# Performance work log

Measured on AMD Instinct MI355X. Metric: run time of the kernel, lower is better.

The kernel has to match this reference:

```python
import jax, jax.numpy as jnp
import numpy as np

H = 4096          # hidden_size (Llama-3.1-8B)
BLK = 32          # sca_block_size
NB = H // BLK     # 128 blocks
R = 4             # sca_block_rank
K = 3             # sca_top_k
SIGMA = 1.0       # sca_sigma
NUM_TASKS = 10


def setup_inputs() -> dict:
    key = jax.random.key(0)
    ks = jax.random.split(key, 9)
    B, S = 4, 4096
    x = jax.random.normal(ks[0], (B, S, H), jnp.float32)
    task_ids = jax.random.randint(ks[1], (B,), 0, NUM_TASKS)
    task_emb = jax.random.normal(ks[2], (NUM_TASKS, H), jnp.float32) * 0.02
    Wp = jax.random.normal(ks[3], (H, 3), jnp.float32) * (1.0 / np.sqrt(H))  # spatial_proj (xavier-ish)
    bp = jnp.zeros((3,), jnp.float32)
    centers = jax.random.normal(ks[4], (NB, 3), jnp.float32)                 # block_centers
    A = jax.random.normal(ks[5], (NB, H, R), jnp.float32) * 0.02             # per-block down proj
    Bm = jax.random.normal(ks[6], (NB, R, BLK), jnp.float32) * 0.02          # per-block up proj into its hidden slice
    adapter_scale = jnp.float32(1.0)
    return dict(x=x, task_ids=task_ids, task_emb=task_emb, Wp=Wp, bp=bp,
                centers=centers, A=A, Bm=Bm, adapter_scale=adapter_scale)


def reference(x, task_ids, task_emb, Wp, bp, centers, A, Bm, adapter_scale):
    # task conditioning
    h = x + task_emb[task_ids][:, None, :]                     # [B,S,H]
    # spatial routing: project tokens to 3D, Gaussian score vs block centers
    coords = h @ Wp + bp                                       # [B,S,3]
    d2 = jnp.sum((coords[:, :, None, :] - centers[None, None]) ** 2, axis=-1)  # [B,S,NB]
    scores = -d2 / (2.0 * SIGMA ** 2)
    top_s, top_i = jax.lax.top_k(scores, K)                    # [B,S,K]
    gates = jax.nn.softmax(top_s, axis=-1)                     # soft mask over selected blocks
    # low-rank adapter per block (dense spmm_impl): down-project against all blocks, gather top-k
    z = jnp.einsum('bsh,nhr->bsnr', h, A)                      # [B,S,NB,R]
    z_sel = jnp.take_along_axis(z, top_i[..., None], axis=2)   # [B,S,K,R]
    B_sel = Bm[top_i]                                          # [B,S,K,R,BLK]
    delta_blk = jnp.einsum('bskr,bskrc->bskc', z_sel, B_sel) * gates[..., None]  # [B,S,K,BLK]
    # scatter block outputs into their hidden slices
    Bn, Sn = x.shape[0], x.shape[1]
    cols = top_i[..., None] * BLK + jnp.arange(BLK)            # [B,S,K,BLK]
    bi = jnp.arange(Bn)[:, None, None, None]
    si = jnp.arange(Sn)[None, :, None, None]
    delta = jnp.zeros_like(x).at[bi, si, cols].add(delta_blk)  # [B,S,H]
    return x + adapter_scale * delta
```

## Files before the change

### kernel.cpp

```cpp
#include <hip/hip_runtime.h>
#include <math.h>

#define HDIM 4096
#define NBLK 128
#define RNK  4
#define TOPK 3

typedef float f4 __attribute__((ext_vector_type(4)));
typedef float f2 __attribute__((ext_vector_type(2)));
typedef _Float16 h8 __attribute__((ext_vector_type(8)));

__global__ __launch_bounds__(256) void convert_A(
    const float* __restrict__ A, _Float16* __restrict__ Ah)
{
    int i = blockIdx.x * 256 + threadIdx.x;
    const f4* src = reinterpret_cast<const f4*>(A);
    f4 a0 = __builtin_nontemporal_load(src + 2 * i);
    f4 a1 = __builtin_nontemporal_load(src + 2 * i + 1);
    h8 r;
    r[0] = (_Float16)a0.x; r[1] = (_Float16)a0.y;
    r[2] = (_Float16)a0.z; r[3] = (_Float16)a0.w;
    r[4] = (_Float16)a1.x; r[5] = (_Float16)a1.y;
    r[6] = (_Float16)a1.z; r[7] = (_Float16)a1.w;
    reinterpret_cast<h8*>(Ah)[i] = r;
}

template<bool FP16A>
__global__ __launch_bounds__(256) void npl_fused(
    const float* __restrict__ x,
    const int*   __restrict__ task_ids,
    const float* __restrict__ task_emb,
    const float* __restrict__ Wp,
    const float* __restrict__ bp,
    const float* __restrict__ centers,
    const float* __restrict__ A,
    const _Float16* __restrict__ Ah,
    const float* __restrict__ Bm,
    const float* __restrict__ scale_p,
    float* __restrict__ out,
    int S_per_batch)
{
    __shared__ float h_lds[HDIM];
    __shared__ float red[4][16];
    __shared__ float sc[NBLK];
    __shared__ float zf[TOPK * RNK];
    __shared__ int   top_i[TOPK];
    __shared__ float gate[TOPK];
    __shared__ float dblk[TOPK * 32];
    __shared__ float coords_s[3];

    const int tid  = threadIdx.x;
    const int wid  = tid >> 6;
    const int lane = tid & 63;
    const int token = blockIdx.x;
    const int b = token / S_per_batch;
    const int task = task_ids[b];

    const float* xrow = x + (size_t)token * HDIM;
    const float* trow = task_emb + (size_t)task * HDIM;
    float*       orow = out + (size_t)token * HDIM;

    const f4* xr4 = reinterpret_cast<const f4*>(xrow);
    const f4* tr4 = reinterpret_cast<const f4*>(trow);
    f4*       or4 = reinterpret_cast<f4*>(orow);

    f4 xv[4];
    float c0 = 0.f, c1 = 0.f, c2 = 0.f;
#pragma unroll
    for (int k = 0; k < 4; ++k) {
        int i4 = tid + k * 256;
        f4 xx = __builtin_nontemporal_load(xr4 + i4);
        f4 tt = tr4[i4];
        xv[k] = xx;
        f4 hh = xx + tt;
        reinterpret_cast<f4*>(h_lds)[i4] = hh;
        int e = i4 * 4;
        const float* wrow = Wp + (size_t)e * 3;
        c0 += hh.x * wrow[0];  c1 += hh.x * wrow[1];  c2 += hh.x * wrow[2];
        c0 += hh.y * wrow[3];  c1 += hh.y * wrow[4];  c2 += hh.y * wrow[5];
        c0 += hh.z * wrow[6];  c1 += hh.z * wrow[7];  c2 += hh.z * wrow[8];
        c0 += hh.w * wrow[9];  c1 += hh.w * wrow[10]; c2 += hh.w * wrow[11];
    }
#pragma unroll
    for (int off = 32; off; off >>= 1) {
        c0 += __shfl_down(c0, off);
        c1 += __shfl_down(c1, off);
        c2 += __shfl_down(c2, off);
    }
    if (lane == 0) { red[wid][0] = c0; red[wid][1] = c1; red[wid][2] = c2; }
    __syncthreads();
    if (tid == 0) {
        coords_s[0] = red[0][0] + red[1][0] + red[2][0] + red[3][0] + bp[0];
        coords_s[1] = red[0][1] + red[1][1] + red[2][1] + red[3][1] + bp[1];
        coords_s[2] = red[0][2] + red[1][2] + red[2][2] + red[3][2] + bp[2];
    }
    __syncthreads();

    if (tid < NBLK) {
        float dx = coords_s[0] - centers[tid * 3 + 0];
        float dy = coords_s[1] - centers[tid * 3 + 1];
        float dz = coords_s[2] - centers[tid * 3 + 2];
        sc[tid] = -0.5f * (dx * dx + dy * dy + dz * dz);
    }
    __syncthreads();

    if (wid == 0) {
        float v1 = sc[lane];
        float v2 = sc[lane + 64];
#pragma unroll
        for (int kk = 0; kk < TOPK; ++kk) {
            float v = v1; int idx = lane;
            if (v2 > v || (v2 == v && (lane + 64) < idx)) { v = v2; idx = lane + 64; }
#pragma unroll
            for (int off = 32; off; off >>= 1) {
                float ov = __shfl_down(v, off);
                int   oi = __shfl_down(idx, off);
                if (ov > v || (ov == v && oi < idx)) { v = ov; idx = oi; }
            }
            idx = __shfl(idx, 0);
            v   = __shfl(v, 0);
            if (lane == 0) { top_i[kk] = idx; gate[kk] = v; }
            if (idx == lane)      v1 = -3.0e38f;
            if (idx == lane + 64) v2 = -3.0e38f;
        }
        if (lane == 0) {
            float m  = gate[0];
            float e0 = 1.0f;
            float e1 = expf(gate[1] - m);
            float e2 = expf(gate[2] - m);
            float inv = 1.0f / (e0 + e1 + e2);
            float s = scale_p[0];
            gate[0] = e0 * inv * s;
            gate[1] = e1 * inv * s;
            gate[2] = e2 * inv * s;
        }
    }
    __syncthreads();

    float zp[TOPK][RNK];
#pragma unroll
    for (int kk = 0; kk < TOPK; ++kk)
#pragma unroll
        for (int r = 0; r < RNK; ++r) zp[kk][r] = 0.f;

    if (FP16A) {
#pragma unroll
        for (int kk = 0; kk < TOPK; ++kk) {
            int n = top_i[kk];
            const h8* Arow = reinterpret_cast<const h8*>(Ah + (size_t)n * HDIM * RNK);
#pragma unroll 4
            for (int j = 0; j < 8; ++j) {
                int idx = tid + j * 256;
                h8 a = Arow[idx];
                f2 hv = reinterpret_cast<const f2*>(h_lds)[idx];
                zp[kk][0] += hv.x * (float)a[0] + hv.y * (float)a[4];
                zp[kk][1] += hv.x * (float)a[1] + hv.y * (float)a[5];
                zp[kk][2] += hv.x * (float)a[2] + hv.y * (float)a[6];
                zp[kk][3] += hv.x * (float)a[3] + hv.y * (float)a[7];
            }
        }
    } else {
#pragma unroll
        for (int kk = 0; kk < TOPK; ++kk) {
            int n = top_i[kk];
            const f4* Arow = reinterpret_cast<const f4*>(A + (size_t)n * HDIM * RNK);
#pragma unroll 4
            for (int k = 0; k < 16; ++k) {
                int i = tid + k * 256;
                f4 a = Arow[i];
                float hv = h_lds[i];
                zp[kk][0] += hv * a.x;
                zp[kk][1] += hv * a.y;
                zp[kk][2] += hv * a.z;
                zp[kk][3] += hv * a.w;
            }
        }
    }
#pragma unroll
    for (int off = 32; off; off >>= 1) {
#pragma unroll
        for (int kk = 0; kk < TOPK; ++kk)
#pragma unroll
            for (int r = 0; r < RNK; ++r)
                zp[kk][r] += __shfl_down(zp[kk][r], off);
    }
    if (lane == 0) {
#pragma unroll
        for (int kk = 0; kk < TOPK; ++kk)
#pragma unroll
            for (int r = 0; r < RNK; ++r)
                red[wid][kk * RNK + r] = zp[kk][r];
    }
    __syncthreads();
    if (tid < TOPK * RNK)
        zf[tid] = red[0][tid] + red[1][tid] + red[2][tid] + red[3][tid];
    __syncthreads();

    if (tid < TOPK * 32) {
        int kk = tid >> 5, c = tid & 31;
        int n = top_i[kk];
        const float* bm = Bm + (size_t)n * RNK * 32;
        float d = zf[kk * 4 + 0] * bm[c]
                + zf[kk * 4 + 1] * bm[32 + c]
                + zf[kk * 4 + 2] * bm[64 + c]
                + zf[kk * 4 + 3] * bm[96 + c];
        dblk[tid] = d * gate[kk];
    }
    __syncthreads();

    int n0 = top_i[0], n1 = top_i[1], n2 = top_i[2];
#pragma unroll
    for (int k = 0; k < 4; ++k) {
        int i4 = tid + k * 256;
        int e = i4 * 4;
        int bb = e >> 5;
        f4 o = xv[k];
        int base = -1;
        if (bb == n0) base = 0 * 32 + (e & 31);
        else if (bb == n1) base = 1 * 32 + (e & 31);
        else if (bb == n2) base = 2 * 32 + (e & 31);
        if (base >= 0) {
            o.x += dblk[base + 0];
            o.y += dblk[base + 1];
            o.z += dblk[base + 2];
            o.w += dblk[base + 3];
        }
        __builtin_nontemporal_store(o, or4 + i4);
    }
}

extern "C" void kernel_launch(void* const* d_in, const int* in_sizes, int n_in,
                              void* d_out, int out_size, void* d_ws, size_t ws_size,
                              hipStream_t stream) {
    const float* x        = (const float*)d_in[0];
    const int*   task_ids = (const int*)  d_in[1];
    const float* task_emb = (const float*)d_in[2];
    const float* Wp       = (const float*)d_in[3];
    const float* bp       = (const float*)d_in[4];
    const float* centers  = (const float*)d_in[5];
    const float* A        = (const float*)d_in[6];
    const float* Bm       = (const float*)d_in[7];
    const float* scale    = (const float*)d_in[8];

    int tokens = in_sizes[0] / HDIM;
    int B      = in_sizes[1];
    int S      = tokens / B;

    const size_t A_elems = (size_t)NBLK * HDIM * RNK;
    const size_t need    = A_elems * sizeof(_Float16);

    if (ws_size >= need) {
        _Float16* Ah = (_Float16*)d_ws;
        convert_A<<<dim3((int)(A_elems / 8 / 256)), dim3(256), 0, stream>>>(A, Ah);
        npl_fused<true><<<dim3(tokens), dim3(256), 0, stream>>>(
            x, task_ids, task_emb, Wp, bp, centers, A, Ah, Bm, scale,
            (float*)d_out, S);
    } else {
        npl_fused<false><<<dim3(tokens), dim3(256), 0, stream>>>(
            x, task_ids, task_emb, Wp, bp, centers, A, (const _Float16*)d_ws, Bm, scale,
            (float*)d_out, S);
    }
}
```

Measured before the change: 231.2 us.

## Compute routing redundantly per wave and remove intermediate block barriers

```diff
diff --git a/kernel.cpp b/kernel.cpp
--- a/kernel.cpp
+++ b/kernel.cpp
@@ -41,13 +41,8 @@
     int S_per_batch)
 {
     __shared__ float h_lds[HDIM];
-    __shared__ float red[4][16];
-    __shared__ float sc[NBLK];
-    __shared__ float zf[TOPK * RNK];
-    __shared__ int   top_i[TOPK];
-    __shared__ float gate[TOPK];
-    __shared__ float dblk[TOPK * 32];
-    __shared__ float coords_s[3];
+    __shared__ float redc[4][4];
+    __shared__ float redz[4][12];
 
     const int tid  = threadIdx.x;
     const int wid  = tid >> 6;
@@ -87,66 +82,62 @@
         c1 += __shfl_down(c1, off);
         c2 += __shfl_down(c2, off);
     }
-    if (lane == 0) { red[wid][0] = c0; red[wid][1] = c1; red[wid][2] = c2; }
+    if (lane == 0) { redc[wid][0] = c0; redc[wid][1] = c1; redc[wid][2] = c2; }
     __syncthreads();
-    if (tid == 0) {
-        coords_s[0] = red[0][0] + red[1][0] + red[2][0] + red[3][0] + bp[0];
-        coords_s[1] = red[0][1] + red[1][1] + red[2][1] + red[3][1] + bp[1];
-        coords_s[2] = red[0][2] + red[1][2] + red[2][2] + red[3][2] + bp[2];
-    }
-    __syncthreads();
-
-    if (tid < NBLK) {
-        float dx = coords_s[0] - centers[tid * 3 + 0];
-        float dy = coords_s[1] - centers[tid * 3 + 1];
-        float dz = coords_s[2] - centers[tid * 3 + 2];
-        sc[tid] = -0.5f * (dx * dx + dy * dy + dz * dz);
-    }
-    __syncthreads();
-
-    if (wid == 0) {
-        float v1 = sc[lane];
-        float v2 = sc[lane + 64];
+
+    c0 = redc[0][0] + redc[1][0] + redc[2][0] + redc[3][0] + bp[0];
+    c1 = redc[0][1] + redc[1][1] + redc[2][1] + redc[3][1] + bp[1];
+    c2 = redc[0][2] + redc[1][2] + redc[2][2] + redc[3][2] + bp[2];
+
+    float dx = c0 - centers[lane * 3 + 0];
+    float dy = c1 - centers[lane * 3 + 1];
+    float dz = c2 - centers[lane * 3 + 2];
+    float v1 = -0.5f * (dx * dx + dy * dy + dz * dz);
+    dx = c0 - centers[(lane + 64) * 3 + 0];
+    dy = c1 - centers[(lane + 64) * 3 + 1];
+    dz = c2 - centers[(lane + 64) * 3 + 2];
+    float v2 = -0.5f * (dx * dx + dy * dy + dz * dz);
+
+    float tv0, tv1, tv2; int n0, n1, n2;
+#pragma unroll
+    for (int kk = 0; kk < TOPK; ++kk) {
+        float v = v1; int idx = lane;
+        if (v2 > v || (v2 == v && (lane + 64) < idx)) { v = v2; idx = lane + 64; }
+#pragma unroll
+        for (int off = 32; off; off >>= 1) {
+            float ov = __shfl_down(v, off);
+            int   oi = __shfl_down(idx, off);
+            if (ov > v || (ov == v && oi < idx)) { v = ov; idx = oi; }
+        }
+        idx = __shfl(idx, 0);
+        v   = __shfl(v, 0);
+        if (kk == 0)      { tv0 = v; n0 = idx; }
+        else if (kk == 1) { tv1 = v; n1 = idx; }
+        else              { tv2 = v; n2 = idx; }
+        if (idx == lane)      v1 = -3.0e38f;
+        if (idx == lane + 64) v2 = -3.0e38f;
+    }
+
+    float m  = tv0;
+    float e0 = 1.0f;
+    float e1 = expf(tv1 - m);
+    float e2 = expf(tv2 - m);
+    float inv = 1.0f / (e0 + e1 + e2);
+    float s = scale_p[0];
+    float g0 = e0 * inv * s;
+    float g1 = e1 * inv * s;
+    float g2 = e2 * inv * s;
+
+    float zp[TOPK][RNK];
+#pragma unroll
+    for (int kk = 0; kk < TOPK; ++kk)
+#pragma unroll
+        for (int r = 0; r < RNK; ++r) zp[kk][r] = 0.f;
+
+    if (FP16A) {
 #pragma unroll
         for (int kk = 0; kk < TOPK; ++kk) {
-            float v = v1; int idx = lane;
-            if (v2 > v || (v2 == v && (lane + 64) < idx)) { v = v2; idx = lane + 64; }
-#pragma unroll
-            for (int off = 32; off; off >>= 1) {
-                float ov = __shfl_down(v, off);
-                int   oi = __shfl_down(idx, off);
-                if (ov > v || (ov == v && oi < idx)) { v = ov; idx = oi; }
-            }
-            idx = __shfl(idx, 0);
-            v   = __shfl(v, 0);
-            if (lane == 0) { top_i[kk] = idx; gate[kk] = v; }
-            if (idx == lane)      v1 = -3.0e38f;
-            if (idx == lane + 64) v2 = -3.0e38f;
-        }
-        if (lane == 0) {
-            float m  = gate[0];
-            float e0 = 1.0f;
-            float e1 = expf(gate[1] - m);
-            float e2 = expf(gate[2] - m);
-            float inv = 1.0f / (e0 + e1 + e2);
-            float s = scale_p[0];
-            gate[0] = e0 * inv * s;
-            gate[1] = e1 * inv * s;
-            gate[2] = e2 * inv * s;
-        }
-    }
-    __syncthreads();
-
-    float zp[TOPK][RNK];
-#pragma unroll
-    for (int kk = 0; kk < TOPK; ++kk)
-#pragma unroll
-        for (int r = 0; r < RNK; ++r) zp[kk][r] = 0.f;
-
-    if (FP16A) {
-#pragma unroll
-        for (int kk = 0; kk < TOPK; ++kk) {
-            int n = top_i[kk];
+            int n = (kk == 0) ? n0 : (kk == 1) ? n1 : n2;
             const h8* Arow = reinterpret_cast<const h8*>(Ah + (size_t)n * HDIM * RNK);
 #pragma unroll 4
             for (int j = 0; j < 8; ++j) {
@@ -162,7 +153,7 @@
     } else {
 #pragma unroll
         for (int kk = 0; kk < TOPK; ++kk) {
-            int n = top_i[kk];
+            int n = (kk == 0) ? n0 : (kk == 1) ? n1 : n2;
             const f4* Arow = reinterpret_cast<const f4*>(A + (size_t)n * HDIM * RNK);
 #pragma unroll 4
             for (int k = 0; k < 16; ++k) {
@@ -189,41 +180,39 @@
         for (int kk = 0; kk < TOPK; ++kk)
 #pragma unroll
             for (int r = 0; r < RNK; ++r)
-                red[wid][kk * RNK + r] = zp[kk][r];
+                redz[wid][kk * RNK + r] = zp[kk][r];
     }
     __syncthreads();
-    if (tid < TOPK * RNK)
-        zf[tid] = red[0][tid] + red[1][tid] + red[2][tid] + red[3][tid];
-    __syncthreads();
-
-    if (tid < TOPK * 32) {
-        int kk = tid >> 5, c = tid & 31;
-        int n = top_i[kk];
-        const float* bm = Bm + (size_t)n * RNK * 32;
-        float d = zf[kk * 4 + 0] * bm[c]
-                + zf[kk * 4 + 1] * bm[32 + c]
-                + zf[kk * 4 + 2] * bm[64 + c]
-                + zf[kk * 4 + 3] * bm[96 + c];
-        dblk[tid] = d * gate[kk];
-    }
-    __syncthreads();
-
-    int n0 = top_i[0], n1 = top_i[1], n2 = top_i[2];
+
+    float zf_[12];
+#pragma unroll
+    for (int t = 0; t < 12; ++t)
+        zf_[t] = redz[0][t] + redz[1][t] + redz[2][t] + redz[3][t];
+
 #pragma unroll
     for (int k = 0; k < 4; ++k) {
         int i4 = tid + k * 256;
         int e = i4 * 4;
         int bb = e >> 5;
         f4 o = xv[k];
-        int base = -1;
-        if (bb == n0) base = 0 * 32 + (e & 31);
-        else if (bb == n1) base = 1 * 32 + (e & 31);
-        else if (bb == n2) base = 2 * 32 + (e & 31);
-        if (base >= 0) {
-            o.x += dblk[base + 0];
-            o.y += dblk[base + 1];
-            o.z += dblk[base + 2];
-            o.w += dblk[base + 3];
+        int kk = (bb == n0) ? 0 : (bb == n1) ? 1 : (bb == n2) ? 2 : -1;
+        if (kk >= 0) {
+            int nn = (kk == 0) ? n0 : (kk == 1) ? n1 : n2;
+            float za = (kk == 0) ? zf_[0] : (kk == 1) ? zf_[4] : zf_[8];
+            float zb = (kk == 0) ? zf_[1] : (kk == 1) ? zf_[5] : zf_[9];
+            float zc = (kk == 0) ? zf_[2] : (kk == 1) ? zf_[6] : zf_[10];
+            float zd = (kk == 0) ? zf_[3] : (kk == 1) ? zf_[7] : zf_[11];
+            float gg = (kk == 0) ? g0 : (kk == 1) ? g1 : g2;
+            const float* bm = Bm + (size_t)nn * 128;
+            int c = e & 31;
+            float d0 = za * bm[c + 0] + zb * bm[32 + c + 0] + zc * bm[64 + c + 0] + zd * bm[96 + c + 0];
+            float d1 = za * bm[c + 1] + zb * bm[32 + c + 1] + zc * bm[64 + c + 1] + zd * bm[96 + c + 1];
+            float d2 = za * bm[c + 2] + zb * bm[32 + c + 2] + zc * bm[64 + c + 2] + zd * bm[96 + c + 2];
+            float d3 = za * bm[c + 3] + zb * bm[32 + c + 3] + zc * bm[64 + c + 3] + zd * bm[96 + c + 3];
+            o.x += d0 * gg;
+            o.y += d1 * gg;
+            o.z += d2 * gg;
+            o.w += d3 * gg;
         }
         __builtin_nontemporal_store(o, or4 + i4);
     }
```

Result: no change. 228.9 us (-1.0%).
